# Kernel optimization log

Measured on AMD Instinct MI355X. Metric: run time of the kernel, lower is better.

## Reference

```python
import jax, jax.numpy as jnp
import numpy as np

NQ, NKV, HD, SW = 32, 8, 64, 512  # n_q_heads, n_kv_heads, head_dim, sliding_window (layer index 0 -> window active)
QM = NQ // NKV


def _rope_tables(L):
    # inv_freq: (1/1024)^linspace over head_dim//4 freqs, padded with head_dim//4 zeros -> head_dim//2
    inv_freq = (1.0 / 1024.0) ** jnp.linspace(0.0, 1.0, HD // 4)
    inv_freq = jnp.concatenate([inv_freq, jnp.zeros(HD // 4)])
    theta = jnp.arange(L, dtype=jnp.float32)[:, None] * inv_freq[None, :]  # (L, HD//2)
    return jnp.cos(theta), jnp.sin(theta)


def _apply_rope(x, cos, sin):
    x1, x2 = jnp.split(x, 2, axis=-1)
    return jnp.concatenate([x1 * cos + x2 * sin, -x1 * sin + x2 * cos], axis=-1)


def setup_inputs() -> dict:
    key = jax.random.key(0)
    k1, k2, k3 = jax.random.split(key, 3)
    B, L, D = 1, 2048, 2048
    x = jax.random.normal(k1, (B, L, D), jnp.float32)
    W_qkv = jax.random.normal(k2, (D, (NQ + 2 * NKV) * HD), jnp.float32) * 0.02
    W_out = jax.random.normal(k3, (NQ * HD, D), jnp.float32) * 0.02
    s = jnp.zeros((1, NKV, QM), jnp.float32)  # attention-sink logits (zero-init param)
    return {"x": x, "W_qkv": W_qkv, "W_out": W_out, "s": s}


def reference(x, W_qkv, W_out, s):
    B, L, D = x.shape
    proj = x @ W_qkv
    q, k, v = jnp.split(proj, (NQ * HD, (NQ + NKV) * HD), axis=-1)
    cos, sin = _rope_tables(L)
    q = _apply_rope(q.reshape(B, L, NKV, QM, HD), cos[None, :, None, None, :], sin[None, :, None, None, :])
    k = _apply_rope(k.reshape(B, L, NKV, HD), cos[None, :, None, :], sin[None, :, None, :])
    v = v.reshape(B, L, NKV, HD)
    sm_scale = 1.0 / jnp.sqrt(jnp.float32(HD))
    # scores: (B, NKV, QM, L, L) -- GQA: K shared across QM query heads (avoids explicit broadcast_to)
    attn = jnp.einsum('bqhmd,bkhd->bhmqk', q, k) * sm_scale
    q_pos = jnp.arange(L)[:, None]
    k_pos = jnp.arange(L)[None, :]
    mask = (q_pos >= k_pos) & (q_pos < k_pos + SW)  # causal AND within sliding window
    # Faithful to source: where(mask, -inf, attn) (mask polarity exactly as in the original module)
    attn = jnp.where(mask, -jnp.inf, attn)
    sink = jnp.broadcast_to(s[:, :, :, None, None], attn.shape[:-1] + (1,))
    w = jax.nn.softmax(jnp.concatenate([attn, sink], axis=-1), axis=-1)[..., :-1]
    out = jnp.einsum('bhmqk,bkhd->bqhmd', w, v).reshape(B, L, NQ * HD)
    return out @ W_out
```

## Files before the change

### kernel.cpp

```cpp
#include <hip/hip_runtime.h>
#include <hip/hip_bf16.h>
#include <math.h>

#define L_SEQ 2048
#define DMODEL 2048
#define PROJW 3072
#define NQH 32
#define NKVH 8
#define HD 64
#define SW 512

typedef __attribute__((ext_vector_type(8))) short bf16x8;
typedef __attribute__((ext_vector_type(4))) float f32x4;

__device__ __forceinline__ ushort f2bf(float x) {
    __hip_bfloat16 h = __float2bfloat16(x);
    return *reinterpret_cast<ushort*>(&h);
}
__device__ __forceinline__ float bf2f(ushort u) {
    __hip_bfloat16 h = *reinterpret_cast<__hip_bfloat16*>(&u);
    return __bfloat162float(h);
}

__device__ __forceinline__ void glds16(const void* g, void* l) {
    __builtin_amdgcn_global_load_lds(
        (__attribute__((address_space(1))) void*)(void*)g,
        (__attribute__((address_space(3))) void*)l, 16, 0, 0);
}

__global__ void rope_tables_kernel(float* __restrict__ cosT, float* __restrict__ sinT) {
    int pos = blockIdx.x * blockDim.x + threadIdx.x;
    if (pos >= L_SEQ) return;
    #pragma unroll
    for (int j = 0; j < 32; ++j) {
        float c, s;
        if (j < 16) {
            float t = (float)j * (1.0f / 15.0f);
            float freq = powf(1.0f / 1024.0f, t);
            float th = (float)pos * freq;
            sincosf(th, &s, &c);
        } else {
            c = 1.0f; s = 0.0f;
        }
        cosT[pos * 32 + j] = c;
        sinT[pos * 32 + j] = s;
    }
}

__global__ __launch_bounds__(256) void split_rm_kernel(const float* __restrict__ A,
                                                       ushort* __restrict__ hi,
                                                       ushort* __restrict__ lo) {
    int i = (blockIdx.x * 256 + threadIdx.x) * 4;
    float4 v = *reinterpret_cast<const float4*>(&A[i]);
    float vv[4] = {v.x, v.y, v.z, v.w};
    ushort h[4], l[4];
    #pragma unroll
    for (int j = 0; j < 4; ++j) {
        h[j] = f2bf(vv[j]);
        l[j] = f2bf(vv[j] - bf2f(h[j]));
    }
    *reinterpret_cast<ushort4*>(&hi[i]) = make_ushort4(h[0], h[1], h[2], h[3]);
    *reinterpret_cast<ushort4*>(&lo[i]) = make_ushort4(l[0], l[1], l[2], l[3]);
}

__global__ __launch_bounds__(256) void split_t_kernel(const float* __restrict__ W,
                                                      ushort* __restrict__ hi,
                                                      ushort* __restrict__ lo,
                                                      int K, int N) {
    __shared__ float t[32][33];
    int n0 = blockIdx.x * 32, k0 = blockIdx.y * 32;
    int tx = threadIdx.x & 31, ty = threadIdx.x >> 5;
    #pragma unroll
    for (int r = 0; r < 32; r += 8)
        t[ty + r][tx] = W[(size_t)(k0 + ty + r) * N + n0 + tx];
    __syncthreads();
    #pragma unroll
    for (int r = 0; r < 32; r += 8) {
        float v = t[tx][ty + r];
        ushort h = f2bf(v);
        ushort l = f2bf(v - bf2f(h));
        size_t o = (size_t)(n0 + ty + r) * K + k0 + tx;
        hi[o] = h;
        lo[o] = l;
    }
}

#define GBK 32

__global__ __launch_bounds__(256) void gemm_bf16x2_kernel(
    const ushort* __restrict__ Ahi, const ushort* __restrict__ Alo,
    const ushort* __restrict__ Bhi, const ushort* __restrict__ Blo,
    float* __restrict__ C, int M, int N, int K)
{
    __shared__ __align__(16) ushort sAh[128 * 32];
    __shared__ __align__(16) ushort sAl[128 * 32];
    __shared__ __align__(16) ushort sBh[128 * 32];
    __shared__ __align__(16) ushort sBl[128 * 32];

    const int tid = threadIdx.x;
    const int w = tid >> 6, lane = tid & 63;
    const int bm = blockIdx.y * 128, bn = blockIdx.x * 128;
    const int wr = w >> 1, wc = w & 1;

    f32x4 acc[4][4];
    #pragma unroll
    for (int i = 0; i < 4; ++i)
        #pragma unroll
        for (int j = 0; j < 4; ++j)
            acc[i][j] = (f32x4){0.0f, 0.0f, 0.0f, 0.0f};

    const int q0 = w * 128 + lane;
    const int q1 = q0 + 64;
    const int r0 = q0 >> 2, r1 = q1 >> 2;
    const int ks0 = ((q0 & 3) ^ (r0 & 3)) * 8;
    const int ks1 = ((q1 & 3) ^ (r1 & 3)) * 8;
    const ushort* gAh0 = Ahi + (size_t)(bm + r0) * K + ks0;
    const ushort* gAh1 = Ahi + (size_t)(bm + r1) * K + ks1;
    const ushort* gAl0 = Alo + (size_t)(bm + r0) * K + ks0;
    const ushort* gAl1 = Alo + (size_t)(bm + r1) * K + ks1;
    const ushort* gBh0 = Bhi + (size_t)(bn + r0) * K + ks0;
    const ushort* gBh1 = Bhi + (size_t)(bn + r1) * K + ks1;
    const ushort* gBl0 = Blo + (size_t)(bn + r0) * K + ks0;
    const ushort* gBl1 = Blo + (size_t)(bn + r1) * K + ks1;
    ushort* dAh0 = sAh + (w * 2 + 0) * 512;
    ushort* dAh1 = sAh + (w * 2 + 1) * 512;
    ushort* dAl0 = sAl + (w * 2 + 0) * 512;
    ushort* dAl1 = sAl + (w * 2 + 1) * 512;
    ushort* dBh0 = sBh + (w * 2 + 0) * 512;
    ushort* dBh1 = sBh + (w * 2 + 1) * 512;
    ushort* dBl0 = sBl + (w * 2 + 0) * 512;
    ushort* dBl1 = sBl + (w * 2 + 1) * 512;

    const int kg = lane >> 4;
    const int fr = lane & 15;

    for (int k0 = 0; k0 < K; k0 += GBK) {
        __syncthreads();
        glds16(gAh0 + k0, dAh0);
        glds16(gAh1 + k0, dAh1);
        glds16(gBh0 + k0, dBh0);
        glds16(gBh1 + k0, dBh1);
        glds16(gAl0 + k0, dAl0);
        glds16(gAl1 + k0, dAl1);
        glds16(gBl0 + k0, dBl0);
        glds16(gBl1 + k0, dBl1);
        __syncthreads();

        bf16x8 ah[4], al[4], bh[4], bl[4];
        #pragma unroll
        for (int i = 0; i < 4; ++i) {
            int row = wr * 64 + i * 16 + fr;
            int off = row * 32 + ((kg ^ (row & 3)) * 8);
            ah[i] = *reinterpret_cast<const bf16x8*>(&sAh[off]);
            al[i] = *reinterpret_cast<const bf16x8*>(&sAl[off]);
        }
        #pragma unroll
        for (int j = 0; j < 4; ++j) {
            int row = wc * 64 + j * 16 + fr;
            int off = row * 32 + ((kg ^ (row & 3)) * 8);
            bh[j] = *reinterpret_cast<const bf16x8*>(&sBh[off]);
            bl[j] = *reinterpret_cast<const bf16x8*>(&sBl[off]);
        }
        #pragma unroll
        for (int i = 0; i < 4; ++i)
            #pragma unroll
            for (int j = 0; j < 4; ++j) {
                acc[i][j] = __builtin_amdgcn_mfma_f32_16x16x32_bf16(ah[i], bh[j], acc[i][j], 0, 0, 0);
                acc[i][j] = __builtin_amdgcn_mfma_f32_16x16x32_bf16(ah[i], bl[j], acc[i][j], 0, 0, 0);
                acc[i][j] = __builtin_amdgcn_mfma_f32_16x16x32_bf16(al[i], bh[j], acc[i][j], 0, 0, 0);
            }
    }

    const int rq = (lane >> 4) * 4;
    #pragma unroll
    for (int i = 0; i < 4; ++i)
        #pragma unroll
        for (int j = 0; j < 4; ++j) {
            #pragma unroll
            for (int q = 0; q < 4; ++q) {
                C[(size_t)(bm + wr * 64 + i * 16 + rq + q) * N + bn + wc * 64 + j * 16 + fr]
                    = acc[i][j][q];
            }
        }
}

__global__ __launch_bounds__(256) void prep_qk_kernel(
    const float* __restrict__ proj,
    const float* __restrict__ cosT, const float* __restrict__ sinT,
    ushort* __restrict__ Qh, ushort* __restrict__ Ql,
    ushort* __restrict__ Kh, ushort* __restrict__ Kl)
{
    int pos = blockIdx.x;
    const float* row = proj + (size_t)pos * PROJW;
    const float* ct = cosT + pos * 32;
    const float* st = sinT + pos * 32;
    int t = threadIdx.x;
    #pragma unroll
    for (int it = 0; it < 4; ++it) {
        int p = t + it * 256;
        int head = p >> 5, d = p & 31;
        float x1 = row[head * HD + d], x2 = row[head * HD + d + 32];
        float c = ct[d], s = st[d];
        float y1 = (x1 * c + x2 * s) * 0.125f;
        float y2 = (-x1 * s + x2 * c) * 0.125f;
        size_t o = ((size_t)head * L_SEQ + pos) * HD + d;
        ushort h1 = f2bf(y1); Qh[o] = h1;      Ql[o] = f2bf(y1 - bf2f(h1));
        ushort h2 = f2bf(y2); Qh[o + 32] = h2; Ql[o + 32] = f2bf(y2 - bf2f(h2));
    }
    {
        int head = t >> 5, d = t & 31;
        float x1 = row[DMODEL + head * HD + d], x2 = row[DMODEL + head * HD + d + 32];
        float c = ct[d], s = st[d];
        float y1 = x1 * c + x2 * s;
        float y2 = -x1 * s + x2 * c;
        size_t o = ((size_t)head * L_SEQ + pos) * HD + d;
        ushort h1 = f2bf(y1); Kh[o] = h1;      Kl[o] = f2bf(y1 - bf2f(h1));
        ushort h2 = f2bf(y2); Kh[o + 32] = h2; Kl[o + 32] = f2bf(y2 - bf2f(h2));
    }
}

__global__ __launch_bounds__(256) void prep_v_kernel(const float* __restrict__ proj,
                                                     ushort* __restrict__ Vth,
                                                     ushort* __restrict__ Vtl)
{
    __shared__ float tile[64][65];
    int h = blockIdx.y, p0 = blockIdx.x * 64;
    int t = threadIdx.x;
    {
        int r = t >> 2, c0 = (t & 3) * 16;
        const float* src = proj + (size_t)(p0 + r) * PROJW + DMODEL + NKVH * HD + h * HD + c0;
        #pragma unroll
        for (int i = 0; i < 16; i += 4) {
            float4 v = *reinterpret_cast<const float4*>(src + i);
            tile[r][c0 + i + 0] = v.x;
            tile[r][c0 + i + 1] = v.y;
            tile[r][c0 + i + 2] = v.z;
            tile[r][c0 + i + 3] = v.w;
        }
    }
    __syncthreads();
    {
        int d = t >> 2, c0 = (t & 3) * 16;
        ushort hh[16], ll[16];
        #pragma unroll
        for (int i = 0; i < 16; ++i) {
            float v = tile[c0 + i][d];
            hh[i] = f2bf(v);
            ll[i] = f2bf(v - bf2f(hh[i]));
        }
        size_t o = ((size_t)h * HD + d) * L_SEQ + p0 + c0;
        #pragma unroll
        for (int i = 0; i < 16; i += 4) {
            *reinterpret_cast<ushort4*>(&Vth[o + i]) = make_ushort4(hh[i], hh[i+1], hh[i+2], hh[i+3]);
            *reinterpret_cast<ushort4*>(&Vtl[o + i]) = make_ushort4(ll[i], ll[i+1], ll[i+2], ll[i+3]);
        }
    }
}

__global__ __launch_bounds__(256, 2) void attn_mfma_kernel(
    const ushort* __restrict__ Qh, const ushort* __restrict__ Ql,
    const ushort* __restrict__ Kh, const ushort* __restrict__ Kl,
    const ushort* __restrict__ Vth, const ushort* __restrict__ Vtl,
    const float* __restrict__ sink,
    ushort* __restrict__ out_hi, ushort* __restrict__ out_lo)
{
    __shared__ __align__(16) ushort KsH[2][4096];
    __shared__ __align__(16) ushort KsL[2][4096];
    __shared__ __align__(16) ushort PtH[4][2048];
    __shared__ __align__(16) ushort PtL[4][2048];

    const int tid = threadIdx.x;
    const int w = tid >> 6, lane = tid & 63;
    const int fr = lane & 15, g = lane >> 4;
    const int bid = blockIdx.x;
    const int h = bid & 7;
    const int q0 = (bid >> 3) * 32;
    const int hq = h * 4 + w;

    const ushort* Qb_h = Qh + ((size_t)hq * L_SEQ + q0) * HD;
    const ushort* Qb_l = Ql + ((size_t)hq * L_SEQ + q0) * HD;
    const ushort* Kb_h = Kh + (size_t)h * L_SEQ * HD;
    const ushort* Kb_l = Kl + (size_t)h * L_SEQ * HD;
    const ushort* Vb_h = Vth + (size_t)h * HD * L_SEQ;
    const ushort* Vb_l = Vtl + (size_t)h * HD * L_SEQ;

    int sA = q0 - 480, sB = q0 - 63;
    int kA = (sA + 63) & ~63; if (kA < 0) kA = 0;
    int kB = sB & ~63;
    bool has_skip = (sB >= 0) && (kA <= kB);
    int n1 = has_skip ? (kA >> 6) : (L_SEQ >> 6);
    int kResume = has_skip ? (kB + 64) : 0;
    int nt = n1 + (has_skip ? ((L_SEQ - kResume) >> 6) : 0);
    #define K0_OF(t) ((t) < n1 ? (t) * 64 : kResume + ((t) - n1) * 64)

    #define STAGE_K(buf, k0s) do {                                                  \
        _Pragma("unroll")                                                           \
        for (int qi = 0; qi < 2; ++qi) {                                            \
            int gq = (w * 2 + qi) * 64 + lane;                                      \
            int srow = gq >> 3, sc = gq & 7;                                        \
            size_t soff = (size_t)((k0s) + srow) * HD + ((sc ^ (srow & 7)) * 8);    \
            glds16(Kb_h + soff, &KsH[buf][(w * 2 + qi) * 512]);                     \
            glds16(Kb_l + soff, &KsL[buf][(w * 2 + qi) * 512]);                     \
        }                                                                           \
    } while (0)

    bf16x8 qbh[2][2], qbl[2][2];
    #pragma unroll
    for (int j = 0; j < 2; ++j)
        #pragma unroll
        for (int kc = 0; kc < 2; ++kc) {
            size_t o = (size_t)(j * 16 + fr) * HD + kc * 32 + g * 8;
            qbh[j][kc] = *reinterpret_cast<const bf16x8*>(Qb_h + o);
            qbl[j][kc] = *reinterpret_cast<const bf16x8*>(Qb_l + o);
        }

    const float sval = sink[hq];
    float m[2] = {sval, sval};
    float l[2] = {1.0f, 1.0f};
    f32x4 ot[4][2];
    #pragma unroll
    for (int i = 0; i < 4; ++i)
        #pragma unroll
        for (int j = 0; j < 2; ++j)
            ot[i][j] = (f32x4){0.0f, 0.0f, 0.0f, 0.0f};

    STAGE_K(0, K0_OF(0));
    __syncthreads();

    for (int t = 0; t < nt; ++t) {
        const int cur = t & 1;
        if (t + 1 < nt) STAGE_K(cur ^ 1, K0_OF(t + 1));
        const int k0 = K0_OF(t);

        bf16x8 kah[4][2], kal[4][2];
        #pragma unroll
        for (int i = 0; i < 4; ++i)
            #pragma unroll
            for (int kc = 0; kc < 2; ++kc) {
                int row = i * 16 + fr;
                int off = row * 64 + (((kc * 4 + g) ^ (row & 7)) * 8);
                kah[i][kc] = *reinterpret_cast<const bf16x8*>(&KsH[cur][off]);
                kal[i][kc] = *reinterpret_cast<const bf16x8*>(&KsL[cur][off]);
            }

        f32x4 st4[4][2];
        #pragma unroll
        for (int i = 0; i < 4; ++i)
            #pragma unroll
            for (int j = 0; j < 2; ++j)
                st4[i][j] = (f32x4){0.0f, 0.0f, 0.0f, 0.0f};
        #pragma unroll
        for (int i = 0; i < 4; ++i)
            #pragma unroll
            for (int j = 0; j < 2; ++j)
                #pragma unroll
                for (int kc = 0; kc < 2; ++kc) {
                    st4[i][j] = __builtin_amdgcn_mfma_f32_16x16x32_bf16(kah[i][kc], qbh[j][kc], st4[i][j], 0, 0, 0);
                    st4[i][j] = __builtin_amdgcn_mfma_f32_16x16x32_bf16(kah[i][kc], qbl[j][kc], st4[i][j], 0, 0, 0);
                    st4[i][j] = __builtin_amdgcn_mfma_f32_16x16x32_bf16(kal[i][kc], qbh[j][kc], st4[i][j], 0, 0, 0);
                }

        bf16x8 vah[4][2], val[4][2];
        #pragma unroll
        for (int i = 0; i < 4; ++i)
            #pragma unroll
            for (int kc = 0; kc < 2; ++kc) {
                size_t o = (size_t)(i * 16 + fr) * L_SEQ + k0 + kc * 32 + g * 8;
                vah[i][kc] = *reinterpret_cast<const bf16x8*>(Vb_h + o);
                val[i][kc] = *reinterpret_cast<const bf16x8*>(Vb_l + o);
            }

        const bool need_mask = (q0 + 31 >= k0) && (q0 < k0 + 63 + SW);

        #pragma unroll
        for (int j = 0; j < 2; ++j) {
            int q = q0 + j * 16 + fr;
            float tm = -INFINITY;
            if (need_mask) {
                #pragma unroll
                for (int i = 0; i < 4; ++i)
                    #pragma unroll
                    for (int r = 0; r < 4; ++r) {
                        int k = k0 + i * 16 + g * 4 + r;
                        float s = st4[i][j][r];
                        if ((q >= k) && (q < k + SW)) s = -INFINITY;
                        st4[i][j][r] = s;
                        tm = fmaxf(tm, s);
                    }
            } else {
                #pragma unroll
                for (int i = 0; i < 4; ++i)
                    #pragma unroll
                    for (int r = 0; r < 4; ++r)
                        tm = fmaxf(tm, st4[i][j][r]);
            }
            tm = fmaxf(tm, __shfl_xor(tm, 16));
            tm = fmaxf(tm, __shfl_xor(tm, 32));
            float nm = fmaxf(m[j], tm);
            float al = __expf(m[j] - nm);
            float ps = 0.0f;
            #pragma unroll
            for (int i = 0; i < 4; ++i)
                #pragma unroll
                for (int r = 0; r < 4; ++r) {
                    float p = __expf(st4[i][j][r] - nm);
                    st4[i][j][r] = p;
                    ps += p;
                }
            ps += __shfl_xor(ps, 16);
            ps += __shfl_xor(ps, 32);
            l[j] = l[j] * al + ps;
            m[j] = nm;
            #pragma unroll
            for (int i = 0; i < 4; ++i) ot[i][j] *= al;

            int prow = j * 16 + fr;
            #pragma unroll
            for (int i = 0; i < 4; ++i) {
                ushort ph[4], pl[4];
                #pragma unroll
                for (int r = 0; r < 4; ++r) {
                    float p = st4[i][j][r];
                    ph[r] = f2bf(p);
                    pl[r] = f2bf(p - bf2f(ph[r]));
                }
                int pc = (i * 2 + (g >> 1)) ^ (prow & 7);
                int poff = prow * 64 + pc * 8 + (g & 1) * 4;
                *reinterpret_cast<ushort4*>(&PtH[w][poff]) = make_ushort4(ph[0], ph[1], ph[2], ph[3]);
                *reinterpret_cast<ushort4*>(&PtL[w][poff]) = make_ushort4(pl[0], pl[1], pl[2], pl[3]);
            }
        }

        bf16x8 pbh[2][2], pbl[2][2];
        #pragma unroll
        for (int j = 0; j < 2; ++j)
            #pragma unroll
            for (int kc = 0; kc < 2; ++kc) {
                int prow = j * 16 + fr;
                int off = prow * 64 + (((kc * 4 + g) ^ (prow & 7)) * 8);
                pbh[j][kc] = *reinterpret_cast<const bf16x8*>(&PtH[w][off]);
                pbl[j][kc] = *reinterpret_cast<const bf16x8*>(&PtL[w][off]);
            }

        #pragma unroll
        for (int i = 0; i < 4; ++i)
            #pragma unroll
            for (int j = 0; j < 2; ++j)
                #pragma unroll
                for (int kc = 0; kc < 2; ++kc) {
                    ot[i][j] = __builtin_amdgcn_mfma_f32_16x16x32_bf16(vah[i][kc], pbh[j][kc], ot[i][j], 0, 0, 0);
                    ot[i][j] = __builtin_amdgcn_mfma_f32_16x16x32_bf16(vah[i][kc], pbl[j][kc], ot[i][j], 0, 0, 0);
                    ot[i][j] = __builtin_amdgcn_mfma_f32_16x16x32_bf16(val[i][kc], pbh[j][kc], ot[i][j], 0, 0, 0);
                }

        __syncthreads();
    }

    #pragma unroll
    for (int j = 0; j < 2; ++j) {
        float inv = 1.0f / l[j];
        int q = q0 + j * 16 + fr;
        #pragma unroll
        for (int i = 0; i < 4; ++i) {
            ushort hh[4], ll[4];
            #pragma unroll
            for (int r = 0; r < 4; ++r) {
                float v = ot[i][j][r] * inv;
                hh[r] = f2bf(v);
                ll[r] = f2bf(v - bf2f(hh[r]));
            }
            size_t o = (size_t)q * DMODEL + hq * HD + i * 16 + g * 4;
            *reinterpret_cast<ushort4*>(&out_hi[o]) = make_ushort4(hh[0], hh[1], hh[2], hh[3]);
            *reinterpret_cast<ushort4*>(&out_lo[o]) = make_ushort4(ll[0], ll[1], ll[2], ll[3]);
        }
    }
    #undef STAGE_K
    #undef K0_OF
}

extern "C" void kernel_launch(void* const* d_in, const int* in_sizes, int n_in,
                              void* d_out, int out_size, void* d_ws, size_t ws_size,
                              hipStream_t stream) {
    const float* x     = (const float*)d_in[0];
    const float* W_qkv = (const float*)d_in[1];
    const float* W_out = (const float*)d_in[2];
    const float* s     = (const float*)d_in[3];
    float* outp = (float*)d_out;

    char* ws = (char*)d_ws;
    float*  proj = (float*)ws;  ws += (size_t)L_SEQ * PROJW * 4;
    float*  cosT = (float*)ws;  ws += (size_t)L_SEQ * 32 * 4;
    float*  sinT = (float*)ws;  ws += (size_t)L_SEQ * 32 * 4;
    ushort* xh   = (ushort*)ws; ws += (size_t)L_SEQ * DMODEL * 2;
    ushort* xl   = (ushort*)ws; ws += (size_t)L_SEQ * DMODEL * 2;
    ushort* wqh  = (ushort*)ws; ws += (size_t)PROJW * DMODEL * 2;
    ushort* wql  = (ushort*)ws; ws += (size_t)PROJW * DMODEL * 2;
    ushort* woh  = (ushort*)ws; ws += (size_t)DMODEL * DMODEL * 2;
    ushort* wol  = (ushort*)ws; ws += (size_t)DMODEL * DMODEL * 2;
    ushort* kh   = (ushort*)ws; ws += (size_t)NKVH * L_SEQ * HD * 2;
    ushort* kl   = (ushort*)ws; ws += (size_t)NKVH * L_SEQ * HD * 2;
    ushort* vth  = (ushort*)ws; ws += (size_t)NKVH * HD * L_SEQ * 2;
    ushort* vtl  = (ushort*)ws; ws += (size_t)NKVH * HD * L_SEQ * 2;

    ushort* qh  = xh;
    ushort* ql  = xl;
    ushort* ath = wqh;
    ushort* atl = wql;

    rope_tables_kernel<<<(L_SEQ + 255) / 256, 256, 0, stream>>>(cosT, sinT);

    split_rm_kernel<<<(L_SEQ * DMODEL) / 1024, 256, 0, stream>>>(x, xh, xl);
    split_t_kernel<<<dim3(PROJW / 32, DMODEL / 32), 256, 0, stream>>>(W_qkv, wqh, wql, DMODEL, PROJW);
    split_t_kernel<<<dim3(DMODEL / 32, DMODEL / 32), 256, 0, stream>>>(W_out, woh, wol, DMODEL, DMODEL);

    gemm_bf16x2_kernel<<<dim3(PROJW / 128, L_SEQ / 128), 256, 0, stream>>>(
        xh, xl, wqh, wql, proj, L_SEQ, PROJW, DMODEL);

    prep_qk_kernel<<<L_SEQ, 256, 0, stream>>>(proj, cosT, sinT, qh, ql, kh, kl);
    prep_v_kernel<<<dim3(L_SEQ / 64, NKVH), 256, 0, stream>>>(proj, vth, vtl);

    attn_mfma_kernel<<<(L_SEQ / 32) * NKVH, 256, 0, stream>>>(
        qh, ql, kh, kl, vth, vtl, s, ath, atl);

    gemm_bf16x2_kernel<<<dim3(DMODEL / 128, L_SEQ / 128), 256, 0, stream>>>(
        ath, atl, woh, wol, outp, L_SEQ, DMODEL, DMODEL);
}
```

Measured before the change: 440.6 us.

## Shrink attention query tile to 16 rows, raise occupancy, add MFMA priority hints

The attention kernel now handles 16 query rows per block instead of 32. This doubles the grid, shrinks the P scratch buffers in shared memory and halves the per-wave accumulator registers, which allows launch bounds of 4 blocks per CU. The P@V product is split into two 32-key chunks, each written to and read back from a smaller swizzled P buffer. s_setprio hints are added around the MFMA bursts. The cost is that each K/V tile staged from global memory now serves only half as many queries, so K and V traffic roughly doubles.

Result: slower. 566.7 us (+28.6%).

```diff
diff --git a/kernel.cpp b/kernel.cpp
--- a/kernel.cpp
+++ b/kernel.cpp
@@ -257,7 +257,7 @@
     }
 }
 
-__global__ __launch_bounds__(256, 2) void attn_mfma_kernel(
+__global__ __launch_bounds__(256, 4) void attn_mfma_kernel(
     const ushort* __restrict__ Qh, const ushort* __restrict__ Ql,
     const ushort* __restrict__ Kh, const ushort* __restrict__ Kl,
     const ushort* __restrict__ Vth, const ushort* __restrict__ Vtl,
@@ -266,15 +266,15 @@
 {
     __shared__ __align__(16) ushort KsH[2][4096];
     __shared__ __align__(16) ushort KsL[2][4096];
-    __shared__ __align__(16) ushort PtH[4][2048];
-    __shared__ __align__(16) ushort PtL[4][2048];
+    __shared__ __align__(16) ushort PtH[4][512];
+    __shared__ __align__(16) ushort PtL[4][512];
 
     const int tid = threadIdx.x;
     const int w = tid >> 6, lane = tid & 63;
     const int fr = lane & 15, g = lane >> 4;
     const int bid = blockIdx.x;
     const int h = bid & 7;
-    const int q0 = (bid >> 3) * 32;
+    const int q0 = (bid >> 3) * 16;
     const int hq = h * 4 + w;
 
     const ushort* Qb_h = Qh + ((size_t)hq * L_SEQ + q0) * HD;
@@ -284,7 +284,7 @@
     const ushort* Vb_h = Vth + (size_t)h * HD * L_SEQ;
     const ushort* Vb_l = Vtl + (size_t)h * HD * L_SEQ;
 
-    int sA = q0 - 480, sB = q0 - 63;
+    int sA = q0 - 496, sB = q0 - 63;
     int kA = (sA + 63) & ~63; if (kA < 0) kA = 0;
     int kB = sB & ~63;
     bool has_skip = (sB >= 0) && (kA <= kB);
@@ -304,25 +304,21 @@
         }                                                                           \
     } while (0)
 
-    bf16x8 qbh[2][2], qbl[2][2];
-    #pragma unroll
-    for (int j = 0; j < 2; ++j)
-        #pragma unroll
-        for (int kc = 0; kc < 2; ++kc) {
-            size_t o = (size_t)(j * 16 + fr) * HD + kc * 32 + g * 8;
-            qbh[j][kc] = *reinterpret_cast<const bf16x8*>(Qb_h + o);
-            qbl[j][kc] = *reinterpret_cast<const bf16x8*>(Qb_l + o);
-        }
+    bf16x8 qbh[2], qbl[2];
+    #pragma unroll
+    for (int kc = 0; kc < 2; ++kc) {
+        size_t o = (size_t)fr * HD + kc * 32 + g * 8;
+        qbh[kc] = *reinterpret_cast<const bf16x8*>(Qb_h + o);
+        qbl[kc] = *reinterpret_cast<const bf16x8*>(Qb_l + o);
+    }
 
     const float sval = sink[hq];
-    float m[2] = {sval, sval};
-    float l[2] = {1.0f, 1.0f};
-    f32x4 ot[4][2];
+    float m = sval;
+    float l = 1.0f;
+    f32x4 ot[4];
     #pragma unroll
     for (int i = 0; i < 4; ++i)
-        #pragma unroll
-        for (int j = 0; j < 2; ++j)
-            ot[i][j] = (f32x4){0.0f, 0.0f, 0.0f, 0.0f};
+        ot[i] = (f32x4){0.0f, 0.0f, 0.0f, 0.0f};
 
     STAGE_K(0, K0_OF(0));
     __syncthreads();
@@ -343,22 +339,20 @@
                 kal[i][kc] = *reinterpret_cast<const bf16x8*>(&KsL[cur][off]);
             }
 
-        f32x4 st4[4][2];
+        f32x4 st4[4];
         #pragma unroll
         for (int i = 0; i < 4; ++i)
-            #pragma unroll
-            for (int j = 0; j < 2; ++j)
-                st4[i][j] = (f32x4){0.0f, 0.0f, 0.0f, 0.0f};
+            st4[i] = (f32x4){0.0f, 0.0f, 0.0f, 0.0f};
+        __builtin_amdgcn_s_setprio(1);
         #pragma unroll
         for (int i = 0; i < 4; ++i)
             #pragma unroll
-            for (int j = 0; j < 2; ++j)
-                #pragma unroll
-                for (int kc = 0; kc < 2; ++kc) {
-                    st4[i][j] = __builtin_amdgcn_mfma_f32_16x16x32_bf16(kah[i][kc], qbh[j][kc], st4[i][j], 0, 0, 0);
-                    st4[i][j] = __builtin_amdgcn_mfma_f32_16x16x32_bf16(kah[i][kc], qbl[j][kc], st4[i][j], 0, 0, 0);
-                    st4[i][j] = __builtin_amdgcn_mfma_f32_16x16x32_bf16(kal[i][kc], qbh[j][kc], st4[i][j], 0, 0, 0);
-                }
+            for (int kc = 0; kc < 2; ++kc) {
+                st4[i] = __builtin_amdgcn_mfma_f32_16x16x32_bf16(kah[i][kc], qbh[kc], st4[i], 0, 0, 0);
+                st4[i] = __builtin_amdgcn_mfma_f32_16x16x32_bf16(kah[i][kc], qbl[kc], st4[i], 0, 0, 0);
+                st4[i] = __builtin_amdgcn_mfma_f32_16x16x32_bf16(kal[i][kc], qbh[kc], st4[i], 0, 0, 0);
+            }
+        __builtin_amdgcn_s_setprio(0);
 
         bf16x8 vah[4][2], val[4][2];
         #pragma unroll
@@ -370,102 +364,90 @@
                 val[i][kc] = *reinterpret_cast<const bf16x8*>(Vb_l + o);
             }
 
-        const bool need_mask = (q0 + 31 >= k0) && (q0 < k0 + 63 + SW);
-
-        #pragma unroll
-        for (int j = 0; j < 2; ++j) {
-            int q = q0 + j * 16 + fr;
-            float tm = -INFINITY;
-            if (need_mask) {
-                #pragma unroll
-                for (int i = 0; i < 4; ++i)
-                    #pragma unroll
-                    for (int r = 0; r < 4; ++r) {
-                        int k = k0 + i * 16 + g * 4 + r;
-                        float s = st4[i][j][r];
-                        if ((q >= k) && (q < k + SW)) s = -INFINITY;
-                        st4[i][j][r] = s;
-                        tm = fmaxf(tm, s);
-                    }
-            } else {
-                #pragma unroll
-                for (int i = 0; i < 4; ++i)
-                    #pragma unroll
-                    for (int r = 0; r < 4; ++r)
-                        tm = fmaxf(tm, st4[i][j][r]);
-            }
-            tm = fmaxf(tm, __shfl_xor(tm, 16));
-            tm = fmaxf(tm, __shfl_xor(tm, 32));
-            float nm = fmaxf(m[j], tm);
-            float al = __expf(m[j] - nm);
-            float ps = 0.0f;
+        const bool need_mask = (q0 + 15 >= k0) && (q0 < k0 + 63 + SW);
+        const int q = q0 + fr;
+
+        float tm = -INFINITY;
+        if (need_mask) {
             #pragma unroll
             for (int i = 0; i < 4; ++i)
                 #pragma unroll
                 for (int r = 0; r < 4; ++r) {
-                    float p = __expf(st4[i][j][r] - nm);
-                    st4[i][j][r] = p;
-                    ps += p;
+                    int k = k0 + i * 16 + g * 4 + r;
+                    float s = st4[i][r];
+                    if ((q >= k) && (q < k + SW)) s = -INFINITY;
+                    st4[i][r] = s;
+                    tm = fmaxf(tm, s);
                 }
-            ps += __shfl_xor(ps, 16);
-            ps += __shfl_xor(ps, 32);
-            l[j] = l[j] * al + ps;
-            m[j] = nm;
-            #pragma unroll
-            for (int i = 0; i < 4; ++i) ot[i][j] *= al;
-
-            int prow = j * 16 + fr;
-            #pragma unroll
-            for (int i = 0; i < 4; ++i) {
+        } else {
+            #pragma unroll
+            for (int i = 0; i < 4; ++i)
+                #pragma unroll
+                for (int r = 0; r < 4; ++r)
+                    tm = fmaxf(tm, st4[i][r]);
+        }
+        tm = fmaxf(tm, __shfl_xor(tm, 16));
+        tm = fmaxf(tm, __shfl_xor(tm, 32));
+        float nm = fmaxf(m, tm);
+        float al = __expf(m - nm);
+        float ps = 0.0f;
+        #pragma unroll
+        for (int i = 0; i < 4; ++i)
+            #pragma unroll
+            for (int r = 0; r < 4; ++r) {
+                float p = __expf(st4[i][r] - nm);
+                st4[i][r] = p;
+                ps += p;
+            }
+        ps += __shfl_xor(ps, 16);
+        ps += __shfl_xor(ps, 32);
+        l = l * al + ps;
+        m = nm;
+        #pragma unroll
+        for (int i = 0; i < 4; ++i) ot[i] *= al;
+
+        #pragma unroll
+        for (int kc = 0; kc < 2; ++kc) {
+            #pragma unroll
+            for (int iLoc = 0; iLoc < 2; ++iLoc) {
+                int i = kc * 2 + iLoc;
                 ushort ph[4], pl[4];
                 #pragma unroll
                 for (int r = 0; r < 4; ++r) {
-                    float p = st4[i][j][r];
+                    float p = st4[i][r];
                     ph[r] = f2bf(p);
                     pl[r] = f2bf(p - bf2f(ph[r]));
                 }
-                int pc = (i * 2 + (g >> 1)) ^ (prow & 7);
-                int poff = prow * 64 + pc * 8 + (g & 1) * 4;
+                int cw = iLoc * 2 + (g >> 1);
+                int poff = fr * 32 + ((cw + fr) & 3) * 8 + (g & 1) * 4;
                 *reinterpret_cast<ushort4*>(&PtH[w][poff]) = make_ushort4(ph[0], ph[1], ph[2], ph[3]);
                 *reinterpret_cast<ushort4*>(&PtL[w][poff]) = make_ushort4(pl[0], pl[1], pl[2], pl[3]);
             }
-        }
-
-        bf16x8 pbh[2][2], pbl[2][2];
-        #pragma unroll
-        for (int j = 0; j < 2; ++j)
-            #pragma unroll
-            for (int kc = 0; kc < 2; ++kc) {
-                int prow = j * 16 + fr;
-                int off = prow * 64 + (((kc * 4 + g) ^ (prow & 7)) * 8);
-                pbh[j][kc] = *reinterpret_cast<const bf16x8*>(&PtH[w][off]);
-                pbl[j][kc] = *reinterpret_cast<const bf16x8*>(&PtL[w][off]);
-            }
-
-        #pragma unroll
-        for (int i = 0; i < 4; ++i)
-            #pragma unroll
-            for (int j = 0; j < 2; ++j)
-                #pragma unroll
-                for (int kc = 0; kc < 2; ++kc) {
-                    ot[i][j] = __builtin_amdgcn_mfma_f32_16x16x32_bf16(vah[i][kc], pbh[j][kc], ot[i][j], 0, 0, 0);
-                    ot[i][j] = __builtin_amdgcn_mfma_f32_16x16x32_bf16(vah[i][kc], pbl[j][kc], ot[i][j], 0, 0, 0);
-                    ot[i][j] = __builtin_amdgcn_mfma_f32_16x16x32_bf16(val[i][kc], pbh[j][kc], ot[i][j], 0, 0, 0);
-                }
+            int roff = fr * 32 + (((g + fr) & 3) * 8);
+            bf16x8 pbh = *reinterpret_cast<const bf16x8*>(&PtH[w][roff]);
+            bf16x8 pbl = *reinterpret_cast<const bf16x8*>(&PtL[w][roff]);
+            __builtin_amdgcn_s_setprio(1);
+            #pragma unroll
+            for (int i = 0; i < 4; ++i) {
+                ot[i] = __builtin_amdgcn_mfma_f32_16x16x32_bf16(vah[i][kc], pbh, ot[i], 0, 0, 0);
+                ot[i] = __builtin_amdgcn_mfma_f32_16x16x32_bf16(vah[i][kc], pbl, ot[i], 0, 0, 0);
+                ot[i] = __builtin_amdgcn_mfma_f32_16x16x32_bf16(val[i][kc], pbh, ot[i], 0, 0, 0);
+            }
+            __builtin_amdgcn_s_setprio(0);
+        }
 
         __syncthreads();
     }
 
-    #pragma unroll
-    for (int j = 0; j < 2; ++j) {
-        float inv = 1.0f / l[j];
-        int q = q0 + j * 16 + fr;
+    {
+        float inv = 1.0f / l;
+        int q = q0 + fr;
         #pragma unroll
         for (int i = 0; i < 4; ++i) {
             ushort hh[4], ll[4];
             #pragma unroll
             for (int r = 0; r < 4; ++r) {
-                float v = ot[i][j][r] * inv;
+                float v = ot[i][r] * inv;
                 hh[r] = f2bf(v);
                 ll[r] = f2bf(v - bf2f(hh[r]));
             }
@@ -519,7 +501,7 @@
     prep_qk_kernel<<<L_SEQ, 256, 0, stream>>>(proj, cosT, sinT, qh, ql, kh, kl);
     prep_v_kernel<<<dim3(L_SEQ / 64, NKVH), 256, 0, stream>>>(proj, vth, vtl);
 
-    attn_mfma_kernel<<<(L_SEQ / 32) * NKVH, 256, 0, stream>>>(
+    attn_mfma_kernel<<<(L_SEQ / 16) * NKVH, 256, 0, stream>>>(
         qh, ql, kh, kl, vth, vtl, s, ath, atl);
 
     gemm_bf16x2_kernel<<<dim3(DMODEL / 128, L_SEQ / 128), 256, 0, stream>>>(
```
